# Performance work log

Measured on AMD Instinct MI355X. Metric: run time of the kernel, lower is better.

The kernel has to match this reference:

```python
import jax, jax.numpy as jnp
import numpy as np

N = 50000
E_RAND = 800000
F_IN = 256
F_OUT = 256
ALPHA = 0.2  # LeakyReLU negative slope


def setup_inputs() -> dict:
    key = jax.random.key(0)
    k1, k2, k3, k4 = jax.random.split(key, 4)
    x = jax.random.normal(k1, (N, F_IN), dtype=jnp.float32)
    # random edges + self-loops so every row has at least one edge (avoids div by 0)
    edge_rand = jax.random.randint(k2, (2, E_RAND), 0, N)
    loops = jnp.arange(N)
    edge = jnp.concatenate([edge_rand, jnp.stack([loops, loops])], axis=1)  # [2, 850000]
    W = jax.random.normal(k3, (F_IN, F_OUT), dtype=jnp.float32) * 0.05
    a = jax.random.normal(k4, (2 * F_OUT,), dtype=jnp.float32) * 0.05
    return {"x": x, "edge": edge, "W": W, "a": a}


def reference(x, edge, W, a):
    # x: [N, F_in], edge: [2, E] (row = dst/aggregation index per torch.sparse.mm(a, h))
    n = x.shape[0]
    f_out = W.shape[1]
    h = x @ W  # [N, F_out]
    src, dst = edge[0], edge[1]
    # a @ [h_src; h_dst] decomposes into two per-node dot products (no [E, 2F] concat)
    s = h @ a[:f_out]   # [N]
    t = h @ a[f_out:]   # [N]
    logit = s[src] + t[dst]                                  # [E]
    e = jnp.exp(-jax.nn.leaky_relu(logit, ALPHA))            # [E]
    rowsum = jax.ops.segment_sum(e, src, num_segments=n)     # [N]
    msg = e[:, None] * h[dst]                                # [E, F_out]
    h_prime = jax.ops.segment_sum(msg, src, num_segments=n)  # [N, F_out]
    h_prime = h_prime / rowsum[:, None]
    return jax.nn.relu(h_prime)  # concat=True path
```

## Files before the change

kernel.cpp:

```cpp
#include <hip/hip_runtime.h>
#include <hip/hip_fp16.h>

#define FDIM 256
#define ALPHA 0.2f

typedef _Float16 half8 __attribute__((ext_vector_type(8)));
typedef float floatx4 __attribute__((ext_vector_type(4)));

__global__ __launch_bounds__(256) void prep_hist(const float* __restrict__ W,
                                                 _Float16* __restrict__ wswz,
                                                 const int* __restrict__ edge,
                                                 int* __restrict__ deg, int E) {
  if (blockIdx.x < 32) {
    const int g = blockIdx.x * 256 + threadIdx.x;
    const int kc = g >> 11, L = g & 2047;
    const int n = L >> 3, c = L & 7;
    half8 hv;
#pragma unroll
    for (int j = 0; j < 8; ++j)
      hv[j] = (_Float16)W[(size_t)(kc * 64 + c * 8 + j) * 256 + n];
    *(half8*)(wswz + (size_t)g * 8) = hv;
  } else {
    const int e = (blockIdx.x - 32) * 256 + threadIdx.x;
    if (e < E) atomicAdd(&deg[edge[e]], 1);
  }
}

#define HT_STRIDE 264
__global__ __launch_bounds__(256) void gemm_mfma(
    const float* __restrict__ x, const _Float16* __restrict__ wswz,
    const float* __restrict__ a, _Float16* __restrict__ h,
    float* __restrict__ s, float* __restrict__ t, int M) {
  __shared__ __align__(16) _Float16 smem[64 * HT_STRIDE];
  _Float16* As = smem;
  const int tid = threadIdx.x;
  const int w = tid >> 6, l = tid & 63;
  const int l15 = l & 15, q = l >> 4;
  const int row0 = blockIdx.x * 64;

  floatx4 acc[4][4];
#pragma unroll
  for (int mt = 0; mt < 4; ++mt)
#pragma unroll
    for (int nt = 0; nt < 4; ++nt) acc[mt][nt] = (floatx4){0.f, 0.f, 0.f, 0.f};

  const int id0 = tid, id1 = 256 + tid;
  const int m0 = id0 >> 3, c0 = (id0 & 7) ^ (m0 & 7);
  const int m1 = id1 >> 3, c1 = (id1 & 7) ^ (m1 & 7);
  const int r0 = row0 + m0, r1 = row0 + m1;

  float4 pf[2][2];
  auto loadA = [&](int kc) {
    pf[0][0] = pf[0][1] = pf[1][0] = pf[1][1] = make_float4(0.f, 0.f, 0.f, 0.f);
    if (r0 < M) {
      const float4* p = (const float4*)(x + (size_t)r0 * 256 + kc * 64 + c0 * 8);
      pf[0][0] = p[0];
      pf[0][1] = p[1];
    }
    if (r1 < M) {
      const float4* p = (const float4*)(x + (size_t)r1 * 256 + kc * 64 + c1 * 8);
      pf[1][0] = p[0];
      pf[1][1] = p[1];
    }
  };
  auto storeA = [&]() {
#pragma unroll
    for (int hf = 0; hf < 2; ++hf) {
      half8 hv;
      hv[0] = (_Float16)pf[hf][0].x; hv[1] = (_Float16)pf[hf][0].y;
      hv[2] = (_Float16)pf[hf][0].z; hv[3] = (_Float16)pf[hf][0].w;
      hv[4] = (_Float16)pf[hf][1].x; hv[5] = (_Float16)pf[hf][1].y;
      hv[6] = (_Float16)pf[hf][1].z; hv[7] = (_Float16)pf[hf][1].w;
      *(half8*)(As + (size_t)(hf * 256 + tid) * 8) = hv;
    }
  };

  loadA(0);
  for (int kc = 0; kc < 4; ++kc) {
    storeA();
    half8 bf[2][4];
#pragma unroll
    for (int ks = 0; ks < 2; ++ks) {
      const int c = ks * 4 + q;
#pragma unroll
      for (int nt = 0; nt < 4; ++nt) {
        const int n = w * 64 + nt * 16 + l15;
        bf[ks][nt] = *(const half8*)(wswz + (size_t)(kc * 2048 + n * 8 + c) * 8);
      }
    }
    __syncthreads();
    if (kc < 3) loadA(kc + 1);
#pragma unroll
    for (int ks = 0; ks < 2; ++ks) {
      const int c = ks * 4 + q;
      half8 af[4];
#pragma unroll
      for (int mt = 0; mt < 4; ++mt) {
        const int m = mt * 16 + l15;
        af[mt] = *(const half8*)(As + (size_t)(m * 8 + (c ^ (m & 7))) * 8);
      }
#pragma unroll
      for (int mt = 0; mt < 4; ++mt)
#pragma unroll
        for (int nt = 0; nt < 4; ++nt)
          acc[mt][nt] = __builtin_amdgcn_mfma_f32_16x16x32_f16(
              af[mt], bf[ks][nt], acc[mt][nt], 0, 0, 0);
    }
    __syncthreads();
  }

#pragma unroll
  for (int mt = 0; mt < 4; ++mt)
#pragma unroll
    for (int nt = 0; nt < 4; ++nt)
#pragma unroll
      for (int r = 0; r < 4; ++r)
        smem[(size_t)(mt * 16 + q * 4 + r) * HT_STRIDE + w * 64 + nt * 16 +
             l15] = (_Float16)acc[mt][nt][r];
  __syncthreads();

  const int w8 = tid >> 5;
  const int colh = (tid & 31) * 8;
#pragma unroll
  for (int p = 0; p < 8; ++p) {
    const int rl = p * 8 + w8;
    const int row = row0 + rl;
    if (row < M)
      *(half8*)(h + (size_t)row * 256 + colh) =
          *(const half8*)(smem + (size_t)rl * HT_STRIDE + colh);
  }

  const int r8 = tid >> 2, seg = tid & 3;
  float sp = 0.f, tp = 0.f;
#pragma unroll
  for (int c8 = 0; c8 < 8; ++c8) {
    const int col = seg * 64 + c8 * 8;
    const half8 hv = *(const half8*)(smem + (size_t)r8 * HT_STRIDE + col);
    const float4 a0 = *(const float4*)(a + col);
    const float4 a1 = *(const float4*)(a + col + 4);
    const float4 b0 = *(const float4*)(a + 256 + col);
    const float4 b1 = *(const float4*)(a + 256 + col + 4);
    sp += (float)hv[0] * a0.x + (float)hv[1] * a0.y + (float)hv[2] * a0.z +
          (float)hv[3] * a0.w + (float)hv[4] * a1.x + (float)hv[5] * a1.y +
          (float)hv[6] * a1.z + (float)hv[7] * a1.w;
    tp += (float)hv[0] * b0.x + (float)hv[1] * b0.y + (float)hv[2] * b0.z +
          (float)hv[3] * b0.w + (float)hv[4] * b1.x + (float)hv[5] * b1.y +
          (float)hv[6] * b1.z + (float)hv[7] * b1.w;
  }
  sp += __shfl_xor(sp, 1);
  sp += __shfl_xor(sp, 2);
  tp += __shfl_xor(tp, 1);
  tp += __shfl_xor(tp, 2);
  if (seg == 0 && row0 + r8 < M) {
    s[row0 + r8] = sp;
    t[row0 + r8] = tp;
  }
}

__global__ __launch_bounds__(1024) void scan1(const int* __restrict__ deg,
                                              int* __restrict__ rowstart,
                                              int* __restrict__ bsum, int n) {
  const int tid = threadIdx.x;
  const int i = blockIdx.x * 1024 + tid;
  const int val = (i < n) ? deg[i] : 0;
  const int lane = tid & 63, wv = tid >> 6;
  int v = val;
#pragma unroll
  for (int off = 1; off < 64; off <<= 1) {
    const int o = __shfl_up(v, off);
    if (lane >= off) v += o;
  }
  __shared__ int wsum[16];
  __shared__ int woff[16];
  if (lane == 63) wsum[wv] = v;
  __syncthreads();
  if (tid < 16) {
    int wv2 = wsum[tid];
#pragma unroll
    for (int off = 1; off < 16; off <<= 1) {
      const int o = __shfl_up(wv2, off);
      if (tid >= off) wv2 += o;
    }
    woff[tid] = wv2;
  }
  __syncthreads();
  const int incl = v + (wv ? woff[wv - 1] : 0);
  if (i < n) rowstart[i] = incl - val;
  if (tid == 1023) bsum[blockIdx.x] = woff[15];
}

__global__ __launch_bounds__(64) void scan2(const int* __restrict__ bsum,
                                            int* __restrict__ boff,
                                            int* __restrict__ rowstart, int nb,
                                            int n) {
  const int tid = threadIdx.x;
  int v = (tid < nb) ? bsum[tid] : 0;
#pragma unroll
  for (int off = 1; off < 64; off <<= 1) {
    const int o = __shfl_up(v, off);
    if (tid >= off) v += o;
  }
  if (tid < nb) boff[tid] = v;
  if (tid == nb - 1) rowstart[n] = v;
}

__global__ __launch_bounds__(1024) void scan3(int* __restrict__ rowstart,
                                              int* __restrict__ rsc,
                                              const int* __restrict__ boff,
                                              int n) {
  const int i = blockIdx.x * 1024 + threadIdx.x;
  if (i < n) {
    const int v = rowstart[i] + (blockIdx.x ? boff[blockIdx.x - 1] : 0);
    rowstart[i] = v;
    rsc[i] = v;
  }
}

__global__ void scatter_kernel(const int* __restrict__ edge,
                               int* __restrict__ rsc,
                               const float* __restrict__ s,
                               const float* __restrict__ t,
                               int2* __restrict__ sde, int E) {
  const int e = blockIdx.x * 256 + threadIdx.x;
  if (e < E) {
    const int src = edge[e];
    const int dst = edge[E + e];
    const float logit = s[src] + t[dst];
    const float lr = logit > 0.f ? logit : ALPHA * logit;
    const float ev = __expf(-lr);
    const int pos = atomicAdd(&rsc[src], 1);
    sde[pos] = make_int2(dst, __float_as_int(ev));
  }
}

__global__ __launch_bounds__(256) void agg_kernel(
    const _Float16* __restrict__ h, const int* __restrict__ rowstart,
    const int2* __restrict__ sde, float* __restrict__ out, int n) {
  const int w = threadIdx.x >> 6, l = threadIdx.x & 63;
  const int row = blockIdx.x * 4 + w;
  if (row >= n) return;
  const int start = rowstart[row], end = rowstart[row + 1];
  const int half = l >> 5;
  const int lh = l & 31;
  const size_t fo = (size_t)lh * 8;
  float acc[8] = {};
  float rs = 0.f;
  int j = start;
  for (; j + 8 <= end; j += 8) {
#pragma unroll
    for (int u = 0; u < 4; ++u) {
      const int2 p = sde[j + u * 2 + half];
      const half8 v = *(const half8*)(h + (size_t)p.x * 256 + fo);
      const float e = __int_as_float(p.y);
      rs += e;
#pragma unroll
      for (int k = 0; k < 8; ++k) acc[k] += e * (float)v[k];
    }
  }
  for (; j < end; j += 2) {
    const int idx = j + half;
    const bool valid = idx < end;
    const int2 p = valid ? sde[idx] : make_int2(0, 0);
    const half8 v = *(const half8*)(h + (size_t)p.x * 256 + fo);
    const float e = valid ? __int_as_float(p.y) : 0.f;
    rs += e;
#pragma unroll
    for (int k = 0; k < 8; ++k) acc[k] += e * (float)v[k];
  }
  rs += __shfl_xor(rs, 32);
#pragma unroll
  for (int k = 0; k < 8; ++k) acc[k] += __shfl_xor(acc[k], 32);
  const float inv = 1.f / rs;
  float4 o;
#pragma unroll
  for (int k = 0; k < 4; ++k) {
    const float vv = acc[half * 4 + k] * inv;
    (&o.x)[k] = vv > 0.f ? vv : 0.f;
  }
  *(float4*)(out + (size_t)row * 256 + lh * 8 + half * 4) = o;
}

extern "C" void kernel_launch(void* const* d_in, const int* in_sizes, int n_in,
                              void* d_out, int out_size, void* d_ws,
                              size_t ws_size, hipStream_t stream) {
  const float* x = (const float*)d_in[0];
  const int* edge = (const int*)d_in[1];
  const float* W = (const float*)d_in[2];
  const float* a = (const float*)d_in[3];
  float* out = (float*)d_out;
  const int N = in_sizes[0] / FDIM;
  const int E = in_sizes[1] / 2;
  const int NB = (N + 1023) / 1024;

  _Float16* h = (_Float16*)d_ws;
  _Float16* wswz = h + (size_t)N * FDIM;
  float* s = (float*)(wswz + 8192 * 8);
  float* t = s + N;
  int* deg = (int*)(t + N);
  int* rsc = deg + N;
  int* rowstart = rsc + N;
  int* bsum = rowstart + N + 2;
  int* boff = bsum + 64;
  int2* sde = (int2*)(boff + 64);

  hipMemsetAsync(deg, 0, (size_t)N * sizeof(int), stream);

  prep_hist<<<32 + (E + 255) / 256, 256, 0, stream>>>(W, wswz, edge, deg, E);
  gemm_mfma<<<(N + 63) / 64, 256, 0, stream>>>(x, wswz, a, h, s, t, N);
  scan1<<<NB, 1024, 0, stream>>>(deg, rowstart, bsum, N);
  scan2<<<1, 64, 0, stream>>>(bsum, boff, rowstart, NB, N);
  scan3<<<NB, 1024, 0, stream>>>(rowstart, rsc, boff, N);
  scatter_kernel<<<(E + 255) / 256, 256, 0, stream>>>(edge, rsc, s, t, sde, E);
  agg_kernel<<<(N + 3) / 4, 256, 0, stream>>>(h, rowstart, sde, out, N);
}
```

Before: 276.4 us.

## Use nontemporal loads/stores for streaming data and software-pipeline aggregation gathers

Edge indices, x, the packed (dst, weight) array and the output are now read or written with nontemporal hints, so that streaming traffic evicts less of the reused h table from cache. The aggregation loop is software-pipelined: the next batch of edge records and their h rows is loaded before the current batch is accumulated, to overlap gather latency with math. This raises register use in agg_kernel and may lower occupancy.

```diff
diff --git a/kernel.cpp b/kernel.cpp
--- a/kernel.cpp
+++ b/kernel.cpp
@@ -6,6 +6,8 @@
 
 typedef _Float16 half8 __attribute__((ext_vector_type(8)));
 typedef float floatx4 __attribute__((ext_vector_type(4)));
+typedef float fltx4 __attribute__((ext_vector_type(4)));
+typedef int intx2 __attribute__((ext_vector_type(2)));
 
 __global__ __launch_bounds__(256) void prep_hist(const float* __restrict__ W,
                                                  _Float16* __restrict__ wswz,
@@ -22,7 +24,7 @@
     *(half8*)(wswz + (size_t)g * 8) = hv;
   } else {
     const int e = (blockIdx.x - 32) * 256 + threadIdx.x;
-    if (e < E) atomicAdd(&deg[edge[e]], 1);
+    if (e < E) atomicAdd(&deg[__builtin_nontemporal_load(edge + e)], 1);
   }
 }
 
@@ -49,28 +51,28 @@
   const int m1 = id1 >> 3, c1 = (id1 & 7) ^ (m1 & 7);
   const int r0 = row0 + m0, r1 = row0 + m1;
 
-  float4 pf[2][2];
+  fltx4 pf[2][2];
   auto loadA = [&](int kc) {
-    pf[0][0] = pf[0][1] = pf[1][0] = pf[1][1] = make_float4(0.f, 0.f, 0.f, 0.f);
+    pf[0][0] = pf[0][1] = pf[1][0] = pf[1][1] = (fltx4){0.f, 0.f, 0.f, 0.f};
     if (r0 < M) {
-      const float4* p = (const float4*)(x + (size_t)r0 * 256 + kc * 64 + c0 * 8);
-      pf[0][0] = p[0];
-      pf[0][1] = p[1];
+      const fltx4* p = (const fltx4*)(x + (size_t)r0 * 256 + kc * 64 + c0 * 8);
+      pf[0][0] = __builtin_nontemporal_load(p);
+      pf[0][1] = __builtin_nontemporal_load(p + 1);
     }
     if (r1 < M) {
-      const float4* p = (const float4*)(x + (size_t)r1 * 256 + kc * 64 + c1 * 8);
-      pf[1][0] = p[0];
-      pf[1][1] = p[1];
+      const fltx4* p = (const fltx4*)(x + (size_t)r1 * 256 + kc * 64 + c1 * 8);
+      pf[1][0] = __builtin_nontemporal_load(p);
+      pf[1][1] = __builtin_nontemporal_load(p + 1);
     }
   };
   auto storeA = [&]() {
 #pragma unroll
     for (int hf = 0; hf < 2; ++hf) {
       half8 hv;
-      hv[0] = (_Float16)pf[hf][0].x; hv[1] = (_Float16)pf[hf][0].y;
-      hv[2] = (_Float16)pf[hf][0].z; hv[3] = (_Float16)pf[hf][0].w;
-      hv[4] = (_Float16)pf[hf][1].x; hv[5] = (_Float16)pf[hf][1].y;
-      hv[6] = (_Float16)pf[hf][1].z; hv[7] = (_Float16)pf[hf][1].w;
+#pragma unroll
+      for (int k4 = 0; k4 < 4; ++k4) hv[k4] = (_Float16)pf[hf][0][k4];
+#pragma unroll
+      for (int k4 = 0; k4 < 4; ++k4) hv[4 + k4] = (_Float16)pf[hf][1][k4];
       *(half8*)(As + (size_t)(hf * 256 + tid) * 8) = hv;
     }
   };
@@ -216,20 +218,22 @@
   }
 }
 
-__global__ void scatter_kernel(const int* __restrict__ edge,
-                               int* __restrict__ rsc,
-                               const float* __restrict__ s,
-                               const float* __restrict__ t,
-                               int2* __restrict__ sde, int E) {
+__global__ __launch_bounds__(256) void scatter_kernel(
+    const int* __restrict__ edge, int* __restrict__ rsc,
+    const float* __restrict__ s, const float* __restrict__ t,
+    int2* __restrict__ sde, int E) {
   const int e = blockIdx.x * 256 + threadIdx.x;
   if (e < E) {
-    const int src = edge[e];
-    const int dst = edge[E + e];
+    const int src = __builtin_nontemporal_load(edge + e);
+    const int dst = __builtin_nontemporal_load(edge + E + e);
     const float logit = s[src] + t[dst];
     const float lr = logit > 0.f ? logit : ALPHA * logit;
     const float ev = __expf(-lr);
     const int pos = atomicAdd(&rsc[src], 1);
-    sde[pos] = make_int2(dst, __float_as_int(ev));
+    intx2 pk;
+    pk.x = dst;
+    pk.y = __float_as_int(ev);
+    __builtin_nontemporal_store(pk, (intx2*)sde + pos);
   }
 }
 
@@ -245,24 +249,56 @@
   const size_t fo = (size_t)lh * 8;
   float acc[8] = {};
   float rs = 0.f;
+  const int cnt = end - start;
   int j = start;
-  for (; j + 8 <= end; j += 8) {
+  const int jend = start + (cnt & ~7);
+  if (j < jend) {
+    intx2 p[4];
+    half8 v[4];
+#pragma unroll
+    for (int u = 0; u < 4; ++u)
+      p[u] = __builtin_nontemporal_load((const intx2*)sde + (j + u * 2 + half));
+#pragma unroll
+    for (int u = 0; u < 4; ++u)
+      v[u] = *(const half8*)(h + (size_t)p[u].x * 256 + fo);
+    j += 8;
+    for (; j < jend; j += 8) {
+      intx2 pn[4];
+      half8 vn[4];
+#pragma unroll
+      for (int u = 0; u < 4; ++u)
+        pn[u] =
+            __builtin_nontemporal_load((const intx2*)sde + (j + u * 2 + half));
+#pragma unroll
+      for (int u = 0; u < 4; ++u)
+        vn[u] = *(const half8*)(h + (size_t)pn[u].x * 256 + fo);
+#pragma unroll
+      for (int u = 0; u < 4; ++u) {
+        const float e = __int_as_float(p[u].y);
+        rs += e;
+#pragma unroll
+        for (int k = 0; k < 8; ++k) acc[k] += e * (float)v[u][k];
+      }
+#pragma unroll
+      for (int u = 0; u < 4; ++u) {
+        p[u] = pn[u];
+        v[u] = vn[u];
+      }
+    }
 #pragma unroll
     for (int u = 0; u < 4; ++u) {
-      const int2 p = sde[j + u * 2 + half];
-      const half8 v = *(const half8*)(h + (size_t)p.x * 256 + fo);
-      const float e = __int_as_float(p.y);
+      const float e = __int_as_float(p[u].y);
       rs += e;
 #pragma unroll
-      for (int k = 0; k < 8; ++k) acc[k] += e * (float)v[k];
+      for (int k = 0; k < 8; ++k) acc[k] += e * (float)v[u][k];
     }
   }
   for (; j < end; j += 2) {
     const int idx = j + half;
     const bool valid = idx < end;
-    const int2 p = valid ? sde[idx] : make_int2(0, 0);
-    const half8 v = *(const half8*)(h + (size_t)p.x * 256 + fo);
-    const float e = valid ? __int_as_float(p.y) : 0.f;
+    int2 pp = valid ? sde[idx] : make_int2(0, 0);
+    const half8 v = *(const half8*)(h + (size_t)pp.x * 256 + fo);
+    const float e = valid ? __int_as_float(pp.y) : 0.f;
     rs += e;
 #pragma unroll
     for (int k = 0; k < 8; ++k) acc[k] += e * (float)v[k];
@@ -271,13 +307,14 @@
 #pragma unroll
   for (int k = 0; k < 8; ++k) acc[k] += __shfl_xor(acc[k], 32);
   const float inv = 1.f / rs;
-  float4 o;
+  fltx4 o;
 #pragma unroll
   for (int k = 0; k < 4; ++k) {
     const float vv = acc[half * 4 + k] * inv;
-    (&o.x)[k] = vv > 0.f ? vv : 0.f;
-  }
-  *(float4*)(out + (size_t)row * 256 + lh * 8 + half * 4) = o;
+    o[k] = vv > 0.f ? vv : 0.f;
+  }
+  __builtin_nontemporal_store(
+      o, (fltx4*)(out + (size_t)row * 256 + lh * 8 + half * 4));
 }
 
 extern "C" void kernel_launch(void* const* d_in, const int* in_sizes, int n_in,
```

Result: slower. 287.6 us (+4.0%).

## Slice h into feature chunks so aggregation gathers stay cache-resident

Applied to the files above, without the earlier changes.

The GEMM now writes h in eight feature slices of 32 halves each (slice-major layout), and the aggregation kernel assigns each block one slice for 64 rows, with four threads per row each covering 8 features. Each slice of h is about 3.2 MB, so the random neighbor gathers for one slice can hit in L2/MALL instead of spanning the full 25 MB table. In exchange, every edge list (sde) is read eight times, once per slice, and each thread walks its row's edges serially with no unrolling. Edge and output accesses use nontemporal loads and stores.

```diff
diff --git a/kernel.cpp b/kernel.cpp
--- a/kernel.cpp
+++ b/kernel.cpp
@@ -6,6 +6,8 @@
 
 typedef _Float16 half8 __attribute__((ext_vector_type(8)));
 typedef float floatx4 __attribute__((ext_vector_type(4)));
+typedef float fltx4 __attribute__((ext_vector_type(4)));
+typedef int intx2 __attribute__((ext_vector_type(2)));
 
 __global__ __launch_bounds__(256) void prep_hist(const float* __restrict__ W,
                                                  _Float16* __restrict__ wswz,
@@ -29,7 +31,7 @@
 #define HT_STRIDE 264
 __global__ __launch_bounds__(256) void gemm_mfma(
     const float* __restrict__ x, const _Float16* __restrict__ wswz,
-    const float* __restrict__ a, _Float16* __restrict__ h,
+    const float* __restrict__ a, _Float16* __restrict__ hs,
     float* __restrict__ s, float* __restrict__ t, int M) {
   __shared__ __align__(16) _Float16 smem[64 * HT_STRIDE];
   _Float16* As = smem;
@@ -121,12 +123,14 @@
 
   const int w8 = tid >> 5;
   const int colh = (tid & 31) * 8;
+  const int sl = colh >> 5;
+  const int cw = colh & 31;
 #pragma unroll
   for (int p = 0; p < 8; ++p) {
     const int rl = p * 8 + w8;
     const int row = row0 + rl;
     if (row < M)
-      *(half8*)(h + (size_t)row * 256 + colh) =
+      *(half8*)(hs + ((size_t)sl * M + row) * 32 + cw) =
           *(const half8*)(smem + (size_t)rl * HT_STRIDE + colh);
   }
 
@@ -234,50 +238,38 @@
 }
 
 __global__ __launch_bounds__(256) void agg_kernel(
-    const _Float16* __restrict__ h, const int* __restrict__ rowstart,
+    const _Float16* __restrict__ hs, const int* __restrict__ rowstart,
     const int2* __restrict__ sde, float* __restrict__ out, int n) {
-  const int w = threadIdx.x >> 6, l = threadIdx.x & 63;
-  const int row = blockIdx.x * 4 + w;
+  const int slice = blockIdx.x & 7;
+  const int rowblk = blockIdx.x >> 3;
+  const int t = threadIdx.x;
+  const int row = rowblk * 64 + (t >> 2);
+  const int fq = t & 3;
   if (row >= n) return;
+  const _Float16* hb = hs + (size_t)slice * n * 32 + fq * 8;
   const int start = rowstart[row], end = rowstart[row + 1];
-  const int half = l >> 5;
-  const int lh = l & 31;
-  const size_t fo = (size_t)lh * 8;
   float acc[8] = {};
   float rs = 0.f;
-  int j = start;
-  for (; j + 8 <= end; j += 8) {
-#pragma unroll
-    for (int u = 0; u < 4; ++u) {
-      const int2 p = sde[j + u * 2 + half];
-      const half8 v = *(const half8*)(h + (size_t)p.x * 256 + fo);
-      const float e = __int_as_float(p.y);
-      rs += e;
-#pragma unroll
-      for (int k = 0; k < 8; ++k) acc[k] += e * (float)v[k];
-    }
-  }
-  for (; j < end; j += 2) {
-    const int idx = j + half;
-    const bool valid = idx < end;
-    const int2 p = valid ? sde[idx] : make_int2(0, 0);
-    const half8 v = *(const half8*)(h + (size_t)p.x * 256 + fo);
-    const float e = valid ? __int_as_float(p.y) : 0.f;
+  for (int j = start; j < end; ++j) {
+    const intx2 p = __builtin_nontemporal_load((const intx2*)sde + j);
+    const float e = __int_as_float(p.y);
     rs += e;
+    const half8 v = *(const half8*)(hb + (size_t)p.x * 32);
 #pragma unroll
     for (int k = 0; k < 8; ++k) acc[k] += e * (float)v[k];
   }
-  rs += __shfl_xor(rs, 32);
-#pragma unroll
-  for (int k = 0; k < 8; ++k) acc[k] += __shfl_xor(acc[k], 32);
   const float inv = 1.f / rs;
-  float4 o;
+  fltx4 o0, o1;
 #pragma unroll
   for (int k = 0; k < 4; ++k) {
-    const float vv = acc[half * 4 + k] * inv;
-    (&o.x)[k] = vv > 0.f ? vv : 0.f;
-  }
-  *(float4*)(out + (size_t)row * 256 + lh * 8 + half * 4) = o;
+    const float v0 = acc[k] * inv;
+    const float v1 = acc[4 + k] * inv;
+    o0[k] = v0 > 0.f ? v0 : 0.f;
+    o1[k] = v1 > 0.f ? v1 : 0.f;
+  }
+  float* op = out + (size_t)row * 256 + slice * 32 + fq * 8;
+  __builtin_nontemporal_store(o0, (fltx4*)op);
+  __builtin_nontemporal_store(o1, (fltx4*)(op + 4));
 }
 
 extern "C" void kernel_launch(void* const* d_in, const int* in_sizes, int n_in,
@@ -292,8 +284,8 @@
   const int E = in_sizes[1] / 2;
   const int NB = (N + 1023) / 1024;
 
-  _Float16* h = (_Float16*)d_ws;
-  _Float16* wswz = h + (size_t)N * FDIM;
+  _Float16* hs = (_Float16*)d_ws;
+  _Float16* wswz = hs + (size_t)N * FDIM;
   float* s = (float*)(wswz + 8192 * 8);
   float* t = s + N;
   int* deg = (int*)(t + N);
@@ -306,10 +298,11 @@
   hipMemsetAsync(deg, 0, (size_t)N * sizeof(int), stream);
 
   prep_hist<<<32 + (E + 255) / 256, 256, 0, stream>>>(W, wswz, edge, deg, E);
-  gemm_mfma<<<(N + 63) / 64, 256, 0, stream>>>(x, wswz, a, h, s, t, N);
+  gemm_mfma<<<(N + 63) / 64, 256, 0, stream>>>(x, wswz, a, hs, s, t, N);
   scan1<<<NB, 1024, 0, stream>>>(deg, rowstart, bsum, N);
   scan2<<<1, 64, 0, stream>>>(bsum, boff, rowstart, NB, N);
   scan3<<<NB, 1024, 0, stream>>>(rowstart, rsc, boff, N);
   scatter_kernel<<<(E + 255) / 256, 256, 0, stream>>>(edge, rsc, s, t, sde, E);
-  agg_kernel<<<(N + 3) / 4, 256, 0, stream>>>(h, rowstart, sde, out, N);
-}
+  agg_kernel<<<((N + 63) / 64) * 8, 256, 0, stream>>>(hs, rowstart, sde, out,
+                                                      N);
+}
```

Result: slower. 378.6 us (+37.0%).

## Move degree histogram into GEMM launch and merge scan stages into one kernel

Applied to the files above, without the earlier changes.

The edge-degree histogram blocks now run as extra blocks of the GEMM kernel instead of with the W-swizzle kernel, so the atomic histogram work overlaps the GEMM. The second and third prefix-scan kernels are fused into a single one-block kernel that computes block offsets in shared memory and applies them to all rows. This removes one launch and the boff buffer. The cost is that the final offset pass now runs in a single 1024-thread block over 50k elements instead of across many blocks.

```diff
diff --git a/kernel.cpp b/kernel.cpp
--- a/kernel.cpp
+++ b/kernel.cpp
@@ -6,31 +6,32 @@
 
 typedef _Float16 half8 __attribute__((ext_vector_type(8)));
 typedef float floatx4 __attribute__((ext_vector_type(4)));
-
-__global__ __launch_bounds__(256) void prep_hist(const float* __restrict__ W,
-                                                 _Float16* __restrict__ wswz,
-                                                 const int* __restrict__ edge,
-                                                 int* __restrict__ deg, int E) {
-  if (blockIdx.x < 32) {
-    const int g = blockIdx.x * 256 + threadIdx.x;
-    const int kc = g >> 11, L = g & 2047;
-    const int n = L >> 3, c = L & 7;
-    half8 hv;
-#pragma unroll
-    for (int j = 0; j < 8; ++j)
-      hv[j] = (_Float16)W[(size_t)(kc * 64 + c * 8 + j) * 256 + n];
-    *(half8*)(wswz + (size_t)g * 8) = hv;
-  } else {
-    const int e = (blockIdx.x - 32) * 256 + threadIdx.x;
-    if (e < E) atomicAdd(&deg[edge[e]], 1);
-  }
+typedef float fltx4 __attribute__((ext_vector_type(4)));
+typedef int intx2 __attribute__((ext_vector_type(2)));
+
+__global__ __launch_bounds__(256) void prep_w(const float* __restrict__ W,
+                                              _Float16* __restrict__ wswz) {
+  const int g = blockIdx.x * 256 + threadIdx.x;
+  const int kc = g >> 11, L = g & 2047;
+  const int n = L >> 3, c = L & 7;
+  half8 hv;
+#pragma unroll
+  for (int j = 0; j < 8; ++j)
+    hv[j] = (_Float16)W[(size_t)(kc * 64 + c * 8 + j) * 256 + n];
+  *(half8*)(wswz + (size_t)g * 8) = hv;
 }
 
 #define HT_STRIDE 264
-__global__ __launch_bounds__(256) void gemm_mfma(
+__global__ __launch_bounds__(256) void gemm_hist(
     const float* __restrict__ x, const _Float16* __restrict__ wswz,
     const float* __restrict__ a, _Float16* __restrict__ h,
-    float* __restrict__ s, float* __restrict__ t, int M) {
+    float* __restrict__ s, float* __restrict__ t, int M,
+    const int* __restrict__ edge, int* __restrict__ deg, int E, int nblk) {
+  if ((int)blockIdx.x >= nblk) {
+    const int e = ((int)blockIdx.x - nblk) * 256 + threadIdx.x;
+    if (e < E) atomicAdd(&deg[edge[e]], 1);
+    return;
+  }
   __shared__ __align__(16) _Float16 smem[64 * HT_STRIDE];
   _Float16* As = smem;
   const int tid = threadIdx.x;
@@ -189,28 +190,26 @@
   if (tid == 1023) bsum[blockIdx.x] = woff[15];
 }
 
-__global__ __launch_bounds__(64) void scan2(const int* __restrict__ bsum,
-                                            int* __restrict__ boff,
-                                            int* __restrict__ rowstart, int nb,
-                                            int n) {
+__global__ __launch_bounds__(1024) void scan23(const int* __restrict__ bsum,
+                                               int* __restrict__ rowstart,
+                                               int* __restrict__ rsc, int nb,
+                                               int n) {
+  __shared__ int boffsh[64];
   const int tid = threadIdx.x;
-  int v = (tid < nb) ? bsum[tid] : 0;
-#pragma unroll
-  for (int off = 1; off < 64; off <<= 1) {
-    const int o = __shfl_up(v, off);
-    if (tid >= off) v += o;
-  }
-  if (tid < nb) boff[tid] = v;
-  if (tid == nb - 1) rowstart[n] = v;
-}
-
-__global__ __launch_bounds__(1024) void scan3(int* __restrict__ rowstart,
-                                              int* __restrict__ rsc,
-                                              const int* __restrict__ boff,
-                                              int n) {
-  const int i = blockIdx.x * 1024 + threadIdx.x;
-  if (i < n) {
-    const int v = rowstart[i] + (blockIdx.x ? boff[blockIdx.x - 1] : 0);
+  if (tid < 64) {
+    int v = (tid < nb) ? bsum[tid] : 0;
+#pragma unroll
+    for (int off = 1; off < 64; off <<= 1) {
+      const int o = __shfl_up(v, off);
+      if (tid >= off) v += o;
+    }
+    boffsh[tid] = v;
+    if (tid == nb - 1) rowstart[n] = v;
+  }
+  __syncthreads();
+  for (int i = tid; i < n; i += 1024) {
+    const int b = i >> 10;
+    const int v = rowstart[i] + (b ? boffsh[b - 1] : 0);
     rowstart[i] = v;
     rsc[i] = v;
   }
@@ -291,6 +290,8 @@
   const int N = in_sizes[0] / FDIM;
   const int E = in_sizes[1] / 2;
   const int NB = (N + 1023) / 1024;
+  const int NBLK_GEMM = (N + 63) / 64;
+  const int NBLK_HIST = (E + 255) / 256;
 
   _Float16* h = (_Float16*)d_ws;
   _Float16* wswz = h + (size_t)N * FDIM;
@@ -300,16 +301,15 @@
   int* rsc = deg + N;
   int* rowstart = rsc + N;
   int* bsum = rowstart + N + 2;
-  int* boff = bsum + 64;
-  int2* sde = (int2*)(boff + 64);
+  int2* sde = (int2*)(bsum + 64);
 
   hipMemsetAsync(deg, 0, (size_t)N * sizeof(int), stream);
 
-  prep_hist<<<32 + (E + 255) / 256, 256, 0, stream>>>(W, wswz, edge, deg, E);
-  gemm_mfma<<<(N + 63) / 64, 256, 0, stream>>>(x, wswz, a, h, s, t, N);
+  prep_w<<<32, 256, 0, stream>>>(W, wswz);
+  gemm_hist<<<NBLK_GEMM + NBLK_HIST, 256, 0, stream>>>(
+      x, wswz, a, h, s, t, N, edge, deg, E, NBLK_GEMM);
   scan1<<<NB, 1024, 0, stream>>>(deg, rowstart, bsum, N);
-  scan2<<<1, 64, 0, stream>>>(bsum, boff, rowstart, NB, N);
-  scan3<<<NB, 1024, 0, stream>>>(rowstart, rsc, boff, N);
+  scan23<<<1, 1024, 0, stream>>>(bsum, rowstart, rsc, NB, N);
   scatter_kernel<<<(E + 255) / 256, 256, 0, stream>>>(edge, rsc, s, t, sde, E);
   agg_kernel<<<(N + 3) / 4, 256, 0, stream>>>(h, rowstart, sde, out, N);
 }
```

After: 271.1 us. About the same (-1.9%).
